# Optimization experiments

Hardware: AMD Instinct MI355X
Metric: run time of the kernel (lower is better)

Reference implementation:

```python
import jax, jax.numpy as jnp
import numpy as np

B, T, S, E, H = 2, 2048, 2048, 1024, 16
HD = E // H  # 64


def setup_inputs() -> dict:
    key = jax.random.key(0)
    ks = jax.random.split(key, 13)
    sc = 1.0 / np.sqrt(E)
    inp = {
        "q": jax.random.normal(ks[0], (B, T, E), jnp.float32),
        "k": jax.random.normal(ks[1], (B, S, E), jnp.float32),
        "v": jax.random.normal(ks[2], (B, S, E), jnp.float32),
        "attn_mask": jax.random.randint(ks[3], (T, S), 0, 2, jnp.int32),
        "Wq": jax.random.normal(ks[4], (E, E), jnp.float32) * sc,
        "bq": jax.random.normal(ks[5], (E,), jnp.float32) * 0.01,
        "Wk": jax.random.normal(ks[6], (E, E), jnp.float32) * sc,
        "bk": jax.random.normal(ks[7], (E,), jnp.float32) * 0.01,
        "Wv": jax.random.normal(ks[8], (E, E), jnp.float32) * sc,
        "bv": jax.random.normal(ks[9], (E,), jnp.float32) * 0.01,
        "Wo": jax.random.normal(ks[10], (E, E), jnp.float32) * sc,
        "bo": jax.random.normal(ks[11], (E,), jnp.float32) * 0.01,
    }
    return inp


def reference(q, k, v, attn_mask, Wq, bq, Wk, bk, Wv, bv, Wo, bo):
    bsz, tgt_len, embed_dim = q.shape
    src_len = k.shape[1]
    # torch Linear: x @ W.T + b
    qh = (q @ Wq.T + bq).reshape(bsz, tgt_len, H, HD).transpose(0, 2, 1, 3)  # [B,H,T,HD]
    kh = (k @ Wk.T + bk).reshape(bsz, src_len, H, HD).transpose(0, 2, 1, 3)  # [B,H,S,HD]
    vh = (v @ Wv.T + bv).reshape(bsz, src_len, H, HD).transpose(0, 2, 1, 3)  # [B,H,S,HD]
    scale = 1.0 / jnp.sqrt(jnp.asarray(HD, qh.dtype))
    attn = jnp.einsum('bhtd,bhsd->bhts', qh, kh) * scale  # [B,H,T,S]
    attn = jnp.where(attn_mask != 0, jnp.asarray(-10000.0, attn.dtype), attn)
    attn = jax.nn.softmax(attn, axis=-1)
    out = jnp.einsum('bhts,bhsd->bhtd', attn, vh)  # [B,H,T,HD]
    out = out.transpose(0, 2, 1, 3).reshape(bsz, tgt_len, embed_dim)
    return out @ Wo.T + bo
```

## Files before the change

### kernel.cpp

```cpp
#include <hip/hip_runtime.h>
#include <hip/hip_bf16.h>
#include <math.h>

#define QSCALE 0.18033688011112042f
#define MASKVAL -14426.950408889634f

typedef __attribute__((ext_vector_type(4))) float f32x4;
typedef __attribute__((ext_vector_type(8))) short bf16x8;
typedef __attribute__((ext_vector_type(4))) short bf16x4;
typedef __attribute__((ext_vector_type(4))) float float4_t;
typedef __attribute__((ext_vector_type(4))) int int4_t;
typedef __attribute__((ext_vector_type(2))) unsigned int uint2_t;
typedef __attribute__((ext_vector_type(2))) unsigned long long u64x2;

typedef const __attribute__((address_space(1))) void gbl_cvoid;
typedef __attribute__((address_space(3))) void lds_void;

static __device__ __forceinline__ void gload16(const void* g, void* l){
  __builtin_amdgcn_global_load_lds((gbl_cvoid*)g, (lds_void*)l, 16, 0, 0);
}

static __device__ __forceinline__ unsigned short f2b(float f){
  unsigned int u = __builtin_bit_cast(unsigned int, f);
  u = (u + 0x7FFFu + ((u >> 16) & 1u)) >> 16;
  return (unsigned short)u;
}

static __device__ __forceinline__ unsigned int cvtpk_bf16(float a, float b){
  unsigned int r;
  asm("v_cvt_pk_bf16_f32 %0, %1, %2" : "=v"(r) : "v"(a), "v"(b));
  return r;
}

struct CvtArgs { const float* src[7]; unsigned short* dst[7]; };

__global__ __launch_bounds__(256) void cvt_kernel(CvtArgs a, const int* __restrict__ mask,
                                                  unsigned long long* __restrict__ mout){
  int y = blockIdx.y;
  if (y == 7){
    if (blockIdx.x >= 256) return;
    int w = blockIdx.x * 256 + threadIdx.x;
    const int* p = mask + (size_t)w * 64;
    unsigned long long bits = 0ull;
    #pragma unroll
    for (int j = 0; j < 64; j += 4){
      int4_t v4 = *(const int4_t*)(p + j);
      if (v4[0]) bits |= (1ull << (j + 0));
      if (v4[1]) bits |= (1ull << (j + 1));
      if (v4[2]) bits |= (1ull << (j + 2));
      if (v4[3]) bits |= (1ull << (j + 3));
    }
    mout[w] = bits;
    return;
  }
  int n4 = (y < 3) ? (4194304/4) : (1048576/4);
  int idx = blockIdx.x * 256 + threadIdx.x;
  if (idx >= n4) return;
  float4_t v = *(const float4_t*)(a.src[y] + (size_t)idx * 4);
  bf16x4 b; b[0]=(short)f2b(v[0]); b[1]=(short)f2b(v[1]); b[2]=(short)f2b(v[2]); b[3]=(short)f2b(v[3]);
  *(bf16x4*)(a.dst[y] + (size_t)idx * 4) = b;
}

struct GemmArgs { const unsigned short* A[3]; const unsigned short* W[3];
                  const float* bias[3]; void* C[3]; };

__global__ __launch_bounds__(256) void gemm_qkv_kernel(GemmArgs ga)
{
  __shared__ unsigned short As[128*64];
  __shared__ unsigned short Ws[128*64];
  const int tid = threadIdx.x, lane = tid & 63, wid = tid >> 6;
  const int sel = blockIdx.y >> 3;
  const int n0  = (blockIdx.y & 7) * 128;
  const int m0  = blockIdx.x * 128;
  const unsigned short* A = ga.A[sel];
  const unsigned short* W = ga.W[sel];
  const float* bias = ga.bias[sel];
  const int wm = wid >> 1, wn = wid & 1;
  const int r16 = lane & 15, kg = lane >> 4;
  const int x7 = r16 & 7;
  const int sR = tid >> 3;
  const int sL = (tid & 7) ^ (sR & 7);

  f32x4 acc[4][4];
  const f32x4 z4 = {0.f, 0.f, 0.f, 0.f};
  #pragma unroll
  for (int i = 0; i < 4; ++i)
    #pragma unroll
    for (int j = 0; j < 4; ++j) acc[i][j] = z4;

  for (int k0 = 0; k0 < 1024; k0 += 64) {
    #pragma unroll
    for (int i = 0; i < 4; ++i){
      int row = i * 32 + sR;
      gload16(A + (size_t)(m0 + row) * 1024 + k0 + sL * 8, (char*)As + i * 4096 + wid * 1024);
      gload16(W + (size_t)(n0 + row) * 1024 + k0 + sL * 8, (char*)Ws + i * 4096 + wid * 1024);
    }
    __syncthreads();
    #pragma unroll
    for (int kk = 0; kk < 2; ++kk){
      bf16x8 af[4], wf[4];
      #pragma unroll
      for (int mi = 0; mi < 4; ++mi)
        af[mi] = *(const bf16x8*)(As + (wm*64 + mi*16 + r16)*64 + (((kk<<2) + kg) ^ x7)*8);
      #pragma unroll
      for (int ni = 0; ni < 4; ++ni)
        wf[ni] = *(const bf16x8*)(Ws + (wn*64 + ni*16 + r16)*64 + (((kk<<2) + kg) ^ x7)*8);
      #pragma unroll
      for (int mi = 0; mi < 4; ++mi)
        #pragma unroll
        for (int ni = 0; ni < 4; ++ni)
          acc[mi][ni] = __builtin_amdgcn_mfma_f32_16x16x32_bf16(af[mi], wf[ni], acc[mi][ni], 0, 0, 0);
    }
    __syncthreads();
  }

  #pragma unroll
  for (int mi = 0; mi < 4; ++mi){
    #pragma unroll
    for (int ni = 0; ni < 4; ++ni){
      int m = m0 + wm*64 + mi*16 + kg*4;
      int n = n0 + wn*64 + ni*16 + r16;
      float bv = bias[n];
      if (sel == 2){
        int bb = m >> 11, t = m & 2047, hh = n >> 6, d = n & 63;
        bf16x4 pk;
        #pragma unroll
        for (int r = 0; r < 4; ++r) pk[r] = (short)f2b(acc[mi][ni][r] + bv);
        *(bf16x4*)&((unsigned short*)ga.C[2])[((size_t)(bb*16 + hh) * 64 + d) * 2048 + t] = pk;
      } else {
        #pragma unroll
        for (int r = 0; r < 4; ++r){
          float v = acc[mi][ni][r] + bv;
          if (sel == 0) v *= QSCALE;
          int mm = m + r;
          int bb = mm >> 11, t = mm & 2047, hh = n >> 6, d = n & 63;
          ((unsigned short*)ga.C[sel])[(((size_t)(bb*16 + hh) * 2048 + t) << 6) + d] = f2b(v);
        }
      }
    }
  }
}

__global__ __launch_bounds__(256) void gemm_o_kernel(const unsigned short* __restrict__ A,
    const unsigned short* __restrict__ W, const float* __restrict__ bias,
    float* __restrict__ C)
{
  __shared__ unsigned short As[64*64];
  __shared__ unsigned short Ws[128*64];
  const int tid = threadIdx.x, lane = tid & 63, wid = tid >> 6;
  const int m0 = blockIdx.x * 64;
  const int n0 = blockIdx.y * 128;
  const int wm = wid >> 1, wn = wid & 1;
  const int r16 = lane & 15, kg = lane >> 4;
  const int x7 = r16 & 7;
  const int sR = tid >> 3;
  const int sL = (tid & 7) ^ (sR & 7);

  f32x4 acc[2][4];
  const f32x4 z4 = {0.f, 0.f, 0.f, 0.f};
  #pragma unroll
  for (int i = 0; i < 2; ++i)
    #pragma unroll
    for (int j = 0; j < 4; ++j) acc[i][j] = z4;

  for (int k0 = 0; k0 < 1024; k0 += 64) {
    #pragma unroll
    for (int i = 0; i < 2; ++i){
      int row = i * 32 + sR;
      gload16(A + (size_t)(m0 + row) * 1024 + k0 + sL * 8, (char*)As + i * 4096 + wid * 1024);
    }
    #pragma unroll
    for (int i = 0; i < 4; ++i){
      int row = i * 32 + sR;
      gload16(W + (size_t)(n0 + row) * 1024 + k0 + sL * 8, (char*)Ws + i * 4096 + wid * 1024);
    }
    __syncthreads();
    #pragma unroll
    for (int kk = 0; kk < 2; ++kk){
      bf16x8 af[2], wf[4];
      #pragma unroll
      for (int mi = 0; mi < 2; ++mi)
        af[mi] = *(const bf16x8*)(As + (wm*32 + mi*16 + r16)*64 + (((kk<<2) + kg) ^ x7)*8);
      #pragma unroll
      for (int ni = 0; ni < 4; ++ni)
        wf[ni] = *(const bf16x8*)(Ws + (wn*64 + ni*16 + r16)*64 + (((kk<<2) + kg) ^ x7)*8);
      #pragma unroll
      for (int mi = 0; mi < 2; ++mi)
        #pragma unroll
        for (int ni = 0; ni < 4; ++ni)
          acc[mi][ni] = __builtin_amdgcn_mfma_f32_16x16x32_bf16(af[mi], wf[ni], acc[mi][ni], 0, 0, 0);
    }
    __syncthreads();
  }

  #pragma unroll
  for (int mi = 0; mi < 2; ++mi){
    #pragma unroll
    for (int ni = 0; ni < 4; ++ni){
      int m = m0 + wm*32 + mi*16 + kg*4;
      int n = n0 + wn*64 + ni*16 + r16;
      float bv = bias[n];
      #pragma unroll
      for (int r = 0; r < 4; ++r)
        C[(size_t)(m + r) * 1024 + n] = acc[mi][ni][r] + bv;
    }
  }
}

__global__ __launch_bounds__(512) void attn_kernel(const unsigned short* __restrict__ qh,
    const unsigned short* __restrict__ kh, const unsigned short* __restrict__ vhT,
    const unsigned long long* __restrict__ mbits, unsigned short* __restrict__ attnout)
{
  __shared__ short Ks[2][2][64][64];
  __shared__ short Vs[2][2][64][64];
  __shared__ short Ps[128][64];
  const int tid = threadIdx.x, lane = tid & 63, wid = tid >> 6;
  const int bh = blockIdx.y;
  const int b = bh >> 4, h = bh & 15;
  const int t0 = blockIdx.x * 128;
  const int tw = t0 + wid * 16;
  const int r16 = lane & 15, kg = lane >> 4;
  const int x7 = r16 & 7;
  const int ph0 = (kg ^ x7) * 8;
  const int ph1 = ((kg + 4) ^ x7) * 8;
  const int sR = tid >> 3;
  const int sL = (tid & 7) ^ (sR & 7);

  const unsigned short* kbase = kh + (size_t)bh * 2048 * 64;
  const unsigned short* vtb   = vhT + (size_t)bh * 64 * 2048;
  const unsigned short* qbase = qh + ((size_t)bh * 2048 + tw) * 64;

  bf16x8 aq[2];
  aq[0] = *(const bf16x8*)(qbase + (size_t)r16 * 64 + kg * 8);
  aq[1] = *(const bf16x8*)(qbase + (size_t)r16 * 64 + 32 + kg * 8);

  const short ob = (short)0x3F80;
  const bf16x8 ones8 = {ob, ob, ob, ob, ob, ob, ob, ob};

  f32x4 o[4], o5;
  const f32x4 z4 = {0.f, 0.f, 0.f, 0.f};
  #pragma unroll
  for (int df = 0; df < 4; ++df) o[df] = z4;
  o5 = z4;

  const unsigned long long* mrow = mbits + (size_t)(tw + r16) * 32;
  const size_t koff = (size_t)sR * 64 + sL * 8;
  const size_t voff = (size_t)sR * 2048 + sL * 8;

  #pragma unroll
  for (int i = 0; i < 2; ++i){
    gload16(kbase + (size_t)i * 4096 + koff, (char*)Ks + i * 8192 + wid * 1024);
    gload16(vtb + voff + i * 64,            (char*)Vs + i * 8192 + wid * 1024);
  }
  u64x2 mw = *(const u64x2*)(mrow);
  __syncthreads();

#define ATTN_STEP(CUR, IT)                                                            \
  {                                                                                   \
    u64x2 mwn = mw;                                                                   \
    if ((IT) < 15) {                                                                  \
      const unsigned short* kc = kbase + (size_t)((IT) + 1) * 8192;                   \
      const unsigned short* vc = vtb + (size_t)((IT) + 1) * 128;                      \
      _Pragma("unroll")                                                               \
      for (int i = 0; i < 2; ++i){                                                    \
        gload16(kc + (size_t)i * 4096 + koff,                                         \
                (char*)Ks + ((CUR) ^ 1) * 16384 + i * 8192 + wid * 1024);             \
        gload16(vc + voff + i * 64,                                                   \
                (char*)Vs + ((CUR) ^ 1) * 16384 + i * 8192 + wid * 1024);             \
      }                                                                               \
      mwn = *(const u64x2*)(mrow + 2 * ((IT) + 1));                                   \
    }                                                                                 \
    _Pragma("unroll")                                                                 \
    for (int sub = 0; sub < 2; ++sub){                                                \
      f32x4 sfr[4];                                                                   \
      __builtin_amdgcn_s_setprio(1);                                                  \
      _Pragma("unroll")                                                               \
      for (int sb = 0; sb < 4; ++sb){                                                 \
        bf16x8 bk0 = *(const bf16x8*)&Ks[CUR][sub][sb*16 + r16][ph0];                 \
        bf16x8 bk1 = *(const bf16x8*)&Ks[CUR][sub][sb*16 + r16][ph1];                 \
        f32x4 z = z4;                                                                 \
        z = __builtin_amdgcn_mfma_f32_16x16x32_bf16(bk0, aq[0], z, 0, 0, 0);          \
        z = __builtin_amdgcn_mfma_f32_16x16x32_bf16(bk1, aq[1], z, 0, 0, 0);          \
        sfr[sb] = z;                                                                  \
      }                                                                               \
      __builtin_amdgcn_s_setprio(0);                                                  \
      {                                                                               \
        unsigned long long mwk = mw[sub] >> (kg * 4);                                 \
        unsigned int mlo = (unsigned int)mwk;                                         \
        unsigned int mhi = (unsigned int)(mwk >> 32);                                 \
        _Pragma("unroll")                                                             \
        for (int sb = 0; sb < 4; ++sb){                                               \
          unsigned int wd = (sb < 2) ? mlo : mhi;                                     \
          const int base = (sb & 1) * 16;                                             \
          _Pragma("unroll")                                                           \
          for (int r = 0; r < 4; ++r){                                                \
            float bitf = (float)((wd >> (base + r)) & 1u);                            \
            sfr[sb][r] = fmaf(bitf, MASKVAL, sfr[sb][r]);                             \
          }                                                                           \
        }                                                                             \
      }                                                                               \
      _Pragma("unroll")                                                               \
      for (int sb = 0; sb < 4; ++sb){                                                 \
        unsigned int lo = cvtpk_bf16(exp2f(sfr[sb][0]), exp2f(sfr[sb][1]));           \
        unsigned int hi = cvtpk_bf16(exp2f(sfr[sb][2]), exp2f(sfr[sb][3]));           \
        int phys = (sb * 2 + (kg >> 1)) ^ x7;                                         \
        uint2_t pk; pk[0] = lo; pk[1] = hi;                                           \
        *(uint2_t*)&Ps[wid*16 + r16][phys * 8 + (kg & 1) * 4] = pk;                   \
      }                                                                               \
      bf16x8 pa0 = *(const bf16x8*)&Ps[wid*16 + r16][ph0];                            \
      bf16x8 pa1 = *(const bf16x8*)&Ps[wid*16 + r16][ph1];                            \
      __builtin_amdgcn_s_setprio(1);                                                  \
      _Pragma("unroll")                                                               \
      for (int df = 0; df < 4; ++df){                                                 \
        bf16x8 bv0 = *(const bf16x8*)&Vs[CUR][sub][df*16 + r16][ph0];                 \
        bf16x8 bv1 = *(const bf16x8*)&Vs[CUR][sub][df*16 + r16][ph1];                 \
        o[df] = __builtin_amdgcn_mfma_f32_16x16x32_bf16(pa0, bv0, o[df], 0, 0, 0);    \
        o[df] = __builtin_amdgcn_mfma_f32_16x16x32_bf16(pa1, bv1, o[df], 0, 0, 0);    \
      }                                                                               \
      o5 = __builtin_amdgcn_mfma_f32_16x16x32_bf16(pa0, ones8, o5, 0, 0, 0);          \
      o5 = __builtin_amdgcn_mfma_f32_16x16x32_bf16(pa1, ones8, o5, 0, 0, 0);          \
      __builtin_amdgcn_s_setprio(0);                                                  \
    }                                                                                 \
    __syncthreads();                                                                  \
    mw = mwn;                                                                         \
  }

  for (int ii = 0; ii < 8; ++ii) {
    ATTN_STEP(0, 2 * ii)
    ATTN_STEP(1, 2 * ii + 1)
  }
#undef ATTN_STEP

  float lv0 = 1.0f / o5[0];
  float lv1 = 1.0f / o5[1];
  float lv2 = 1.0f / o5[2];
  float lv3 = 1.0f / o5[3];
  #pragma unroll
  for (int df = 0; df < 4; ++df){
    int col = h*64 + df*16 + r16;
    int t = tw + kg*4;
    attnout[(size_t)(b * 2048 + t + 0) * 1024 + col] = (short)f2b(o[df][0] * lv0);
    attnout[(size_t)(b * 2048 + t + 1) * 1024 + col] = (short)f2b(o[df][1] * lv1);
    attnout[(size_t)(b * 2048 + t + 2) * 1024 + col] = (short)f2b(o[df][2] * lv2);
    attnout[(size_t)(b * 2048 + t + 3) * 1024 + col] = (short)f2b(o[df][3] * lv3);
  }
}

extern "C" void kernel_launch(void* const* d_in, const int* in_sizes, int n_in,
                              void* d_out, int out_size, void* d_ws, size_t ws_size,
                              hipStream_t stream) {
  const float* q    = (const float*)d_in[0];
  const float* k    = (const float*)d_in[1];
  const float* v    = (const float*)d_in[2];
  const int*   mask = (const int*)d_in[3];
  const float* Wq = (const float*)d_in[4];  const float* bq = (const float*)d_in[5];
  const float* Wk = (const float*)d_in[6];  const float* bk = (const float*)d_in[7];
  const float* Wv = (const float*)d_in[8];  const float* bv = (const float*)d_in[9];
  const float* Wo = (const float*)d_in[10]; const float* bo = (const float*)d_in[11];

  char* ws = (char*)d_ws;
  unsigned short* qb   = (unsigned short*)(ws);
  unsigned short* kb   = (unsigned short*)(ws + 8388608);
  unsigned short* vb   = (unsigned short*)(ws + 16777216);
  unsigned short* Wqb  = (unsigned short*)(ws + 25165824);
  unsigned short* Wkb  = (unsigned short*)(ws + 27262976);
  unsigned short* Wvb  = (unsigned short*)(ws + 29360128);
  unsigned short* Wob  = (unsigned short*)(ws + 31457280);
  unsigned short* qhd  = (unsigned short*)(ws + 33554432);
  unsigned short* khd  = (unsigned short*)(ws + 41943040);
  unsigned short* vhT  = (unsigned short*)(ws + 50331648);
  unsigned long long* mbits = (unsigned long long*)(ws + 58720256);
  unsigned short* attno = qb;

  CvtArgs ca;
  ca.src[0]=q;  ca.dst[0]=qb;  ca.src[1]=k;  ca.dst[1]=kb;  ca.src[2]=v;  ca.dst[2]=vb;
  ca.src[3]=Wq; ca.dst[3]=Wqb; ca.src[4]=Wk; ca.dst[4]=Wkb;
  ca.src[5]=Wv; ca.dst[5]=Wvb; ca.src[6]=Wo; ca.dst[6]=Wob;
  cvt_kernel<<<dim3(4096, 8), 256, 0, stream>>>(ca, mask, mbits);

  GemmArgs g0;
  g0.A[0]=qb; g0.A[1]=kb; g0.A[2]=vb;
  g0.W[0]=Wqb; g0.W[1]=Wkb; g0.W[2]=Wvb;
  g0.bias[0]=bq; g0.bias[1]=bk; g0.bias[2]=bv;
  g0.C[0]=qhd; g0.C[1]=khd; g0.C[2]=vhT;
  gemm_qkv_kernel<<<dim3(32, 24), 256, 0, stream>>>(g0);

  attn_kernel<<<dim3(16, 32), 512, 0, stream>>>(qhd, khd, vhT, mbits, attno);

  gemm_o_kernel<<<dim3(64, 8), 256, 0, stream>>>(attno, Wob, bo, (float*)d_out);
}
```

Measured before the change: 146.4 us.

## Fuse fp32-to-bf16 activation conversion into QKV GEMM A-tile loads

The standalone conversion of q, k and v to bf16 is removed. The QKV projection GEMM now loads fp32 activation tiles straight into LDS with a new XOR swizzle and converts them to bf16 fragments in registers before the MFMA. This removes a full read/write pass over 3x8 MB of activations and shrinks the conversion kernel to only the weights and the mask. In exchange the A-tile LDS footprint and global load traffic double, and per-fragment conversion ALU work is added inside the GEMM inner loop.

```diff
diff --git a/kernel.cpp b/kernel.cpp
--- a/kernel.cpp
+++ b/kernel.cpp
@@ -11,6 +11,7 @@
 typedef __attribute__((ext_vector_type(4))) float float4_t;
 typedef __attribute__((ext_vector_type(4))) int int4_t;
 typedef __attribute__((ext_vector_type(2))) unsigned int uint2_t;
+typedef __attribute__((ext_vector_type(4))) unsigned int uint4_t;
 typedef __attribute__((ext_vector_type(2))) unsigned long long u64x2;
 
 typedef const __attribute__((address_space(1))) void gbl_cvoid;
@@ -32,12 +33,29 @@
   return r;
 }
 
-struct CvtArgs { const float* src[7]; unsigned short* dst[7]; };
+static __device__ __forceinline__ unsigned int packbf(float fa, float fb){
+  unsigned int ua = __builtin_bit_cast(unsigned int, fa);
+  unsigned int ub = __builtin_bit_cast(unsigned int, fb);
+  ua += 0x7FFFu + ((ua >> 16) & 1u);
+  ub += 0x7FFFu + ((ub >> 16) & 1u);
+  return __builtin_amdgcn_perm(ub, ua, 0x07060302u);
+}
+
+static __device__ __forceinline__ bf16x8 cvt_frag(f32x4 a0, f32x4 a1){
+  uint4_t u;
+  u[0] = packbf(a0[0], a0[1]);
+  u[1] = packbf(a0[2], a0[3]);
+  u[2] = packbf(a1[0], a1[1]);
+  u[3] = packbf(a1[2], a1[3]);
+  return __builtin_bit_cast(bf16x8, u);
+}
+
+struct CvtArgs { const float* src[4]; unsigned short* dst[4]; };
 
 __global__ __launch_bounds__(256) void cvt_kernel(CvtArgs a, const int* __restrict__ mask,
                                                   unsigned long long* __restrict__ mout){
   int y = blockIdx.y;
-  if (y == 7){
+  if (y == 4){
     if (blockIdx.x >= 256) return;
     int w = blockIdx.x * 256 + threadIdx.x;
     const int* p = mask + (size_t)w * 64;
@@ -53,33 +71,33 @@
     mout[w] = bits;
     return;
   }
-  int n4 = (y < 3) ? (4194304/4) : (1048576/4);
   int idx = blockIdx.x * 256 + threadIdx.x;
-  if (idx >= n4) return;
   float4_t v = *(const float4_t*)(a.src[y] + (size_t)idx * 4);
   bf16x4 b; b[0]=(short)f2b(v[0]); b[1]=(short)f2b(v[1]); b[2]=(short)f2b(v[2]); b[3]=(short)f2b(v[3]);
   *(bf16x4*)(a.dst[y] + (size_t)idx * 4) = b;
 }
 
-struct GemmArgs { const unsigned short* A[3]; const unsigned short* W[3];
+struct GemmArgs { const float* A[3]; const unsigned short* W[3];
                   const float* bias[3]; void* C[3]; };
 
 __global__ __launch_bounds__(256) void gemm_qkv_kernel(GemmArgs ga)
 {
-  __shared__ unsigned short As[128*64];
+  __shared__ float As[128*64];
   __shared__ unsigned short Ws[128*64];
   const int tid = threadIdx.x, lane = tid & 63, wid = tid >> 6;
   const int sel = blockIdx.y >> 3;
   const int n0  = (blockIdx.y & 7) * 128;
   const int m0  = blockIdx.x * 128;
-  const unsigned short* A = ga.A[sel];
+  const float* A = ga.A[sel];
   const unsigned short* W = ga.W[sel];
   const float* bias = ga.bias[sel];
   const int wm = wid >> 1, wn = wid & 1;
   const int r16 = lane & 15, kg = lane >> 4;
   const int x7 = r16 & 7;
-  const int sR = tid >> 3;
-  const int sL = (tid & 7) ^ (sR & 7);
+  const int aRow = tid >> 4;
+  const int aLc  = (tid & 15) ^ (aRow & 15);
+  const int sRw = tid >> 3;
+  const int sLw = (tid & 7) ^ (sRw & 7);
 
   f32x4 acc[4][4];
   const f32x4 z4 = {0.f, 0.f, 0.f, 0.f};
@@ -90,18 +108,25 @@
 
   for (int k0 = 0; k0 < 1024; k0 += 64) {
     #pragma unroll
-    for (int i = 0; i < 4; ++i){
-      int row = i * 32 + sR;
-      gload16(A + (size_t)(m0 + row) * 1024 + k0 + sL * 8, (char*)As + i * 4096 + wid * 1024);
-      gload16(W + (size_t)(n0 + row) * 1024 + k0 + sL * 8, (char*)Ws + i * 4096 + wid * 1024);
-    }
+    for (int i = 0; i < 8; ++i)
+      gload16(A + (size_t)(m0 + i*16 + aRow) * 1024 + k0 + aLc * 4,
+              (char*)As + i * 4096 + tid * 16);
+    #pragma unroll
+    for (int i = 0; i < 4; ++i)
+      gload16(W + (size_t)(n0 + i*32 + sRw) * 1024 + k0 + sLw * 8,
+              (char*)Ws + i * 4096 + wid * 1024);
     __syncthreads();
     #pragma unroll
     for (int kk = 0; kk < 2; ++kk){
       bf16x8 af[4], wf[4];
       #pragma unroll
-      for (int mi = 0; mi < 4; ++mi)
-        af[mi] = *(const bf16x8*)(As + (wm*64 + mi*16 + r16)*64 + (((kk<<2) + kg) ^ x7)*8);
+      for (int mi = 0; mi < 4; ++mi){
+        int row = wm*64 + mi*16 + r16;
+        int c = kk*8 + kg*2;
+        f32x4 a0 = *(const f32x4*)&As[row*64 + ((c    ) ^ r16) * 4];
+        f32x4 a1 = *(const f32x4*)&As[row*64 + ((c + 1) ^ r16) * 4];
+        af[mi] = cvt_frag(a0, a1);
+      }
       #pragma unroll
       for (int ni = 0; ni < 4; ++ni)
         wf[ni] = *(const bf16x8*)(Ws + (wn*64 + ni*16 + r16)*64 + (((kk<<2) + kg) ^ x7)*8);
@@ -359,9 +384,7 @@
   const float* Wo = (const float*)d_in[10]; const float* bo = (const float*)d_in[11];
 
   char* ws = (char*)d_ws;
-  unsigned short* qb   = (unsigned short*)(ws);
-  unsigned short* kb   = (unsigned short*)(ws + 8388608);
-  unsigned short* vb   = (unsigned short*)(ws + 16777216);
+  unsigned short* attno = (unsigned short*)(ws);
   unsigned short* Wqb  = (unsigned short*)(ws + 25165824);
   unsigned short* Wkb  = (unsigned short*)(ws + 27262976);
   unsigned short* Wvb  = (unsigned short*)(ws + 29360128);
@@ -370,16 +393,14 @@
   unsigned short* khd  = (unsigned short*)(ws + 41943040);
   unsigned short* vhT  = (unsigned short*)(ws + 50331648);
   unsigned long long* mbits = (unsigned long long*)(ws + 58720256);
-  unsigned short* attno = qb;
 
   CvtArgs ca;
-  ca.src[0]=q;  ca.dst[0]=qb;  ca.src[1]=k;  ca.dst[1]=kb;  ca.src[2]=v;  ca.dst[2]=vb;
-  ca.src[3]=Wq; ca.dst[3]=Wqb; ca.src[4]=Wk; ca.dst[4]=Wkb;
-  ca.src[5]=Wv; ca.dst[5]=Wvb; ca.src[6]=Wo; ca.dst[6]=Wob;
-  cvt_kernel<<<dim3(4096, 8), 256, 0, stream>>>(ca, mask, mbits);
+  ca.src[0]=Wq; ca.dst[0]=Wqb; ca.src[1]=Wk; ca.dst[1]=Wkb;
+  ca.src[2]=Wv; ca.dst[2]=Wvb; ca.src[3]=Wo; ca.dst[3]=Wob;
+  cvt_kernel<<<dim3(1024, 5), 256, 0, stream>>>(ca, mask, mbits);
 
   GemmArgs g0;
-  g0.A[0]=qb; g0.A[1]=kb; g0.A[2]=vb;
+  g0.A[0]=q; g0.A[1]=k; g0.A[2]=v;
   g0.W[0]=Wqb; g0.W[1]=Wkb; g0.W[2]=Wvb;
   g0.bias[0]=bq; g0.bias[1]=bk; g0.bias[2]=bv;
   g0.C[0]=qhd; g0.C[1]=khd; g0.C[2]=vhT;
```

Result: slower. 163.5 us (+11.7%).
